# Performance work log

Measured on AMD Instinct MI355X. Metric: run time of the kernel, lower is better.

The kernel has to match this reference:

```python
import jax, jax.numpy as jnp
import numpy as np

D_MODEL = 1024
NUM_HEADS = 16
D_K = D_MODEL // NUM_HEADS


def setup_inputs() -> dict:
    key = jax.random.key(0)
    ks = jax.random.split(key, 9)
    s = 1.0 / np.sqrt(D_MODEL)
    inp = {"x": jax.random.normal(ks[0], (4, 2048, D_MODEL), dtype=jnp.float32)}
    for i, name in enumerate(["q", "k", "v", "o"]):
        inp[f"W_{name}"] = jax.random.uniform(ks[1 + 2 * i], (D_MODEL, D_MODEL), minval=-s, maxval=s, dtype=jnp.float32)
        inp[f"b_{name}"] = jax.random.uniform(ks[2 + 2 * i], (D_MODEL,), minval=-s, maxval=s, dtype=jnp.float32)
    return inp


def reference(x, W_q, b_q, W_k, b_k, W_v, b_v, W_o, b_o):
    B, S, _ = x.shape
    # torch Linear: y = x @ W.T + b ; reshape to [B, H, S, d_k]
    def proj(W, b):
        return (x @ W.T + b).reshape(B, S, NUM_HEADS, D_K).transpose(0, 2, 1, 3)

    Q, K, V = proj(W_q, b_q), proj(W_k, b_k), proj(W_v, b_v)
    scores = jnp.einsum("bhqd,bhkd->bhqk", Q, K) / np.sqrt(D_K).astype(np.float32)
    # additive causal mask: -inf above diagonal
    causal = jnp.triu(jnp.full((S, S), -jnp.inf, dtype=scores.dtype), k=1)
    scores = scores + causal
    attn = jax.nn.softmax(scores, axis=-1)
    attn = jnp.nan_to_num(attn, nan=0.0)
    # dropout is identity in eval mode
    out = jnp.einsum("bhqk,bhkd->bhqd", attn, V)
    out = out.transpose(0, 2, 1, 3).reshape(B, S, D_MODEL)
    return out @ W_o.T + b_o
```

## Files before the change

### kernel.cpp

```cpp
#include <hip/hip_runtime.h>
#include <hip/hip_bf16.h>
#include <stdint.h>

#define D_MODEL 1024
#define SEQ     2048
#define NH      16
#define DK      64
#define PSTR    72

typedef __bf16 bf16x8 __attribute__((ext_vector_type(8)));
typedef float  f32x4  __attribute__((ext_vector_type(4)));
typedef unsigned short u16;

#define CFENCE() asm volatile("" ::: "memory")

__device__ __forceinline__ u16 f2bf(float f) {
    uint32_t u = __float_as_uint(f);
    u += 0x7FFFu + ((u >> 16) & 1u);
    return (u16)(u >> 16);
}

__device__ __forceinline__ void gl2lds16(const u16* g, u16* l) {
    __builtin_amdgcn_global_load_lds(
        (const __attribute__((address_space(1))) uint32_t*)g,
        (__attribute__((address_space(3))) uint32_t*)l, 16, 0, 0);
}

__global__ __launch_bounds__(256) void cvt_kernel(const float* __restrict__ src,
                                                  u16* __restrict__ dst, int n4) {
    int i = blockIdx.x * blockDim.x + threadIdx.x;
    if (i >= n4) return;
    float4 v = reinterpret_cast<const float4*>(src)[i];
    ushort4 o;
    o.x = f2bf(v.x); o.y = f2bf(v.y); o.z = f2bf(v.z); o.w = f2bf(v.w);
    reinterpret_cast<ushort4*>(dst)[i] = o;
}

__global__ __launch_bounds__(256) void cvt4_kernel(
    const float* __restrict__ s0, const float* __restrict__ s1,
    const float* __restrict__ s2, const float* __restrict__ s3,
    u16* __restrict__ d0, u16* __restrict__ d1,
    u16* __restrict__ d2, u16* __restrict__ d3, int n4) {
    int z = blockIdx.y;
    const float* s = (z == 0) ? s0 : (z == 1) ? s1 : (z == 2) ? s2 : s3;
    u16* d = (z == 0) ? d0 : (z == 1) ? d1 : (z == 2) ? d2 : d3;
    int i = blockIdx.x * blockDim.x + threadIdx.x;
    if (i >= n4) return;
    float4 v = reinterpret_cast<const float4*>(s)[i];
    ushort4 o;
    o.x = f2bf(v.x); o.y = f2bf(v.y); o.z = f2bf(v.z); o.w = f2bf(v.w);
    reinterpret_cast<ushort4*>(d)[i] = o;
}

__device__ __forceinline__ void gemm128_body(const u16* __restrict__ Ag,
                                             const u16* __restrict__ Bg,
                                             u16* As, u16* Bs, f32x4 acc[4][4]) {
    const int K = D_MODEL;
    int tid = threadIdx.x, wave = tid >> 6, lane = tid & 63;
    int l15 = lane & 15, quad = lane >> 4;
    int srow = lane >> 2;
    int scol = (lane & 3) * 8;
    int arg4 = (wave >> 1) * 4;
    int brg4 = (wave & 1) * 4;
#pragma unroll 1
    for (int kc = 0; kc < K; kc += 64) {
        __syncthreads();
#pragma unroll
        for (int j = 0; j < 4; ++j) {
            int p = wave * 4 + j;
            int rg = p >> 1, h = p & 1;
            int row = rg * 16 + srow;
            int col = kc + h * 32 + scol;
            gl2lds16(Ag + row * K + col, As + p * 512);
            gl2lds16(Bg + row * K + col, Bs + p * 512);
        }
        __syncthreads();
#pragma unroll
        for (int h = 0; h < 2; ++h) {
            bf16x8 af[4], bfr[4];
#pragma unroll
            for (int s = 0; s < 4; ++s) {
                af[s]  = *reinterpret_cast<const bf16x8*>(
                    As + ((arg4 + s) * 2 + h) * 512 + l15 * 32 + quad * 8);
                bfr[s] = *reinterpret_cast<const bf16x8*>(
                    Bs + ((brg4 + s) * 2 + h) * 512 + l15 * 32 + quad * 8);
            }
#pragma unroll
            for (int ms = 0; ms < 4; ++ms)
#pragma unroll
                for (int ns = 0; ns < 4; ++ns)
                    acc[ms][ns] = __builtin_amdgcn_mfma_f32_16x16x32_bf16(
                        af[ms], bfr[ns], acc[ms][ns], 0, 0, 0);
        }
    }
}

__device__ __forceinline__ void stage_half(const u16* __restrict__ gb, u16* ls,
                                           int w2, int srow, int scol) {
#pragma unroll
    for (int i = 0; i < 2; ++i)
        gl2lds16(gb + ((w2 + i) * 8 + srow) * D_MODEL + scol,
                 ls + (w2 + i) * 512);
}

__global__ __launch_bounds__(512, 2) void qkv_gemm256(
    const u16* __restrict__ xb,
    const u16* __restrict__ Wq, const u16* __restrict__ Wk, const u16* __restrict__ Wv,
    const float* __restrict__ bq, const float* __restrict__ bk, const float* __restrict__ bv,
    u16* __restrict__ qo, u16* __restrict__ ko, u16* __restrict__ vto) {
    __shared__ __align__(16) u16 smA[2][2][8192];
    __shared__ __align__(16) u16 smB[2][2][8192];
    int z = blockIdx.z;
    const u16* W = (z == 0) ? Wq : (z == 1) ? Wk : Wv;
    const float* bias = (z == 0) ? bq : (z == 1) ? bk : bv;
    int tid = threadIdx.x;
    int lane = tid & 63, wave = tid >> 6;
    int l15 = lane & 15, quad = lane >> 4;
    int wr = wave >> 2, wc = wave & 3;
    int w2 = wave * 2;
    const u16* Abase = xb + (size_t)blockIdx.x * 256 * D_MODEL;
    const u16* Bbase = W + (size_t)blockIdx.y * 256 * D_MODEL;

    int srow = lane >> 3;
    int scol = ((lane & 7) ^ (lane >> 3)) * 8;
    int xb_ = (l15 & 7) << 4;
    int c0 = ((quad * 16) ^ xb_) >> 1;
    int c1 = ((64 + quad * 16) ^ xb_) >> 1;
    int rb0 = (wc & 1) * 64;

    f32x4 acc[8][4];
#pragma unroll
    for (int m = 0; m < 8; ++m)
#pragma unroll
        for (int n = 0; n < 4; ++n) acc[m][n] = (f32x4){0.f, 0.f, 0.f, 0.f};

    stage_half(Abase, &smA[0][0][0], w2, srow, scol);
    stage_half(Abase + 128 * D_MODEL, &smA[0][1][0], w2, srow, scol);
    stage_half(Bbase, &smB[0][0][0], w2, srow, scol);
    stage_half(Bbase + 128 * D_MODEL, &smB[0][1][0], w2, srow, scol);
    stage_half(Abase + 64, &smA[1][0][0], w2, srow, scol);
    asm volatile("s_waitcnt vmcnt(2)" ::: "memory");
    __builtin_amdgcn_s_barrier();
    CFENCE();

#pragma unroll 1
    for (int t = 0; t < 16; ++t) {
        const int p = t & 1;
        const u16* As = &smA[p][wr][0];
        const u16* Bs = &smB[p][wc >> 1][0];
        bf16x8 af[4][2], bfr[4][2];

#pragma unroll
        for (int m = 0; m < 4; ++m) {
            af[m][0] = *reinterpret_cast<const bf16x8*>(As + (m * 16 + l15) * 64 + c0);
            af[m][1] = *reinterpret_cast<const bf16x8*>(As + (m * 16 + l15) * 64 + c1);
        }
#pragma unroll
        for (int nn = 0; nn < 2; ++nn) {
            bfr[nn][0] = *reinterpret_cast<const bf16x8*>(Bs + (rb0 + nn * 16 + l15) * 64 + c0);
            bfr[nn][1] = *reinterpret_cast<const bf16x8*>(Bs + (rb0 + nn * 16 + l15) * 64 + c1);
        }
        if (t < 15) stage_half(Abase + 128 * D_MODEL + (t + 1) * 64,
                               &smA[(t + 1) & 1][1][0], w2, srow, scol);
        CFENCE(); __builtin_amdgcn_s_barrier(); CFENCE();
        __builtin_amdgcn_s_setprio(1);
#pragma unroll
        for (int m = 0; m < 4; ++m)
#pragma unroll
            for (int nn = 0; nn < 2; ++nn) {
                acc[m][nn] = __builtin_amdgcn_mfma_f32_16x16x32_bf16(af[m][0], bfr[nn][0], acc[m][nn], 0, 0, 0);
                acc[m][nn] = __builtin_amdgcn_mfma_f32_16x16x32_bf16(af[m][1], bfr[nn][1], acc[m][nn], 0, 0, 0);
            }
        __builtin_amdgcn_s_setprio(0);
        CFENCE(); __builtin_amdgcn_s_barrier(); CFENCE();

#pragma unroll
        for (int nn = 0; nn < 2; ++nn) {
            bfr[2 + nn][0] = *reinterpret_cast<const bf16x8*>(Bs + (rb0 + (2 + nn) * 16 + l15) * 64 + c0);
            bfr[2 + nn][1] = *reinterpret_cast<const bf16x8*>(Bs + (rb0 + (2 + nn) * 16 + l15) * 64 + c1);
        }
        if (t < 15) stage_half(Bbase + (t + 1) * 64,
                               &smB[(t + 1) & 1][0][0], w2, srow, scol);
        CFENCE(); __builtin_amdgcn_s_barrier(); CFENCE();
        __builtin_amdgcn_s_setprio(1);
#pragma unroll
        for (int m = 0; m < 4; ++m)
#pragma unroll
            for (int nn = 0; nn < 2; ++nn) {
                acc[m][2 + nn] = __builtin_amdgcn_mfma_f32_16x16x32_bf16(af[m][0], bfr[2 + nn][0], acc[m][2 + nn], 0, 0, 0);
                acc[m][2 + nn] = __builtin_amdgcn_mfma_f32_16x16x32_bf16(af[m][1], bfr[2 + nn][1], acc[m][2 + nn], 0, 0, 0);
            }
        __builtin_amdgcn_s_setprio(0);
        CFENCE(); __builtin_amdgcn_s_barrier(); CFENCE();

#pragma unroll
        for (int m = 0; m < 4; ++m) {
            af[m][0] = *reinterpret_cast<const bf16x8*>(As + ((m + 4) * 16 + l15) * 64 + c0);
            af[m][1] = *reinterpret_cast<const bf16x8*>(As + ((m + 4) * 16 + l15) * 64 + c1);
        }
        if (t < 15) stage_half(Bbase + 128 * D_MODEL + (t + 1) * 64,
                               &smB[(t + 1) & 1][1][0], w2, srow, scol);
        CFENCE(); __builtin_amdgcn_s_barrier(); CFENCE();
        __builtin_amdgcn_s_setprio(1);
#pragma unroll
        for (int m = 0; m < 4; ++m)
#pragma unroll
            for (int nn = 0; nn < 2; ++nn) {
                acc[4 + m][nn] = __builtin_amdgcn_mfma_f32_16x16x32_bf16(af[m][0], bfr[nn][0], acc[4 + m][nn], 0, 0, 0);
                acc[4 + m][nn] = __builtin_amdgcn_mfma_f32_16x16x32_bf16(af[m][1], bfr[nn][1], acc[4 + m][nn], 0, 0, 0);
            }
        __builtin_amdgcn_s_setprio(0);
        CFENCE(); __builtin_amdgcn_s_barrier(); CFENCE();

        if (t < 14) stage_half(Abase + (t + 2) * 64,
                               &smA[p][0][0], w2, srow, scol);
        CFENCE(); __builtin_amdgcn_s_barrier(); CFENCE();
        __builtin_amdgcn_s_setprio(1);
#pragma unroll
        for (int m = 0; m < 4; ++m)
#pragma unroll
            for (int nn = 0; nn < 2; ++nn) {
                acc[4 + m][2 + nn] = __builtin_amdgcn_mfma_f32_16x16x32_bf16(af[m][0], bfr[2 + nn][0], acc[4 + m][2 + nn], 0, 0, 0);
                acc[4 + m][2 + nn] = __builtin_amdgcn_mfma_f32_16x16x32_bf16(af[m][1], bfr[2 + nn][1], acc[4 + m][2 + nn], 0, 0, 0);
            }
        __builtin_amdgcn_s_setprio(0);
        if (t < 14) {
            asm volatile("s_waitcnt vmcnt(2)" ::: "memory");
            __builtin_amdgcn_s_barrier(); CFENCE();
        } else if (t == 14) {
            asm volatile("s_waitcnt vmcnt(0)" ::: "memory");
            __builtin_amdgcn_s_barrier(); CFENCE();
        }
    }

    int mw = blockIdx.x * 256 + wr * 128;
    int nwb = blockIdx.y * 256 + wc * 64;
    int hq = (nwb >> 6) & (NH - 1);
    const float qscale = 0.125f * 1.4426950408889634f;

    if (z != 2) {
        u16* dst = (z == 0) ? qo : ko;
        float sc = (z == 0) ? qscale : 1.0f;
        u16* tw = &smA[0][0][0] + wave * 1152;
        float bv0 = bias[nwb + 0 * 16 + l15];
        float bv1 = bias[nwb + 1 * 16 + l15];
        float bv2 = bias[nwb + 2 * 16 + l15];
        float bv3 = bias[nwb + 3 * 16 + l15];
#pragma unroll
        for (int mf = 0; mf < 8; ++mf) {
#pragma unroll
            for (int nf = 0; nf < 4; ++nf) {
                int c = nf * 16 + l15;
                float bv_ = (nf == 0) ? bv0 : (nf == 1) ? bv1 : (nf == 2) ? bv2 : bv3;
#pragma unroll
                for (int r = 0; r < 4; ++r) {
                    int w = quad * 4 + r;
                    tw[w * 72 + (((c >> 3) ^ (w & 7)) << 3) + (c & 7)] =
                        f2bf((acc[mf][nf][r] + bv_) * sc);
                }
            }
            asm volatile("s_waitcnt lgkmcnt(0)" ::: "memory");
#pragma unroll
            for (int i = 0; i < 2; ++i) {
                int w = i * 8 + (lane >> 3);
                bf16x8 vv = *reinterpret_cast<const bf16x8*>(
                    tw + w * 72 + (((lane & 7) ^ (w & 7)) << 3));
                int sg = mw + mf * 16 + w;
                int b = sg >> 11, ss = sg & (SEQ - 1);
                *reinterpret_cast<bf16x8*>(
                    &dst[((b * NH + hq) * SEQ + ss) * DK + (lane & 7) * 8]) = vv;
            }
            asm volatile("s_waitcnt lgkmcnt(0)" ::: "memory");
        }
    } else {
        u16* tw = &smA[0][0][0] + wave * 4608;
        float bv0 = bias[nwb + 0 * 16 + l15];
        float bv1 = bias[nwb + 1 * 16 + l15];
        float bv2 = bias[nwb + 2 * 16 + l15];
        float bv3 = bias[nwb + 3 * 16 + l15];
#pragma unroll
        for (int half = 0; half < 2; ++half) {
#pragma unroll
            for (int mfi = 0; mfi < 4; ++mfi) {
                int mf = half * 4 + mfi;
#pragma unroll
                for (int nf = 0; nf < 4; ++nf) {
                    int w = nf * 16 + l15;
                    float bv_ = (nf == 0) ? bv0 : (nf == 1) ? bv1 : (nf == 2) ? bv2 : bv3;
                    int sl = mfi * 16 + quad * 4;
                    ushort4 pk;
                    pk.x = f2bf(acc[mf][nf][0] + bv_);
                    pk.y = f2bf(acc[mf][nf][1] + bv_);
                    pk.z = f2bf(acc[mf][nf][2] + bv_);
                    pk.w = f2bf(acc[mf][nf][3] + bv_);
                    *reinterpret_cast<ushort4*>(
                        tw + w * 72 + (((sl >> 3) ^ (w & 7)) << 3) + (sl & 7)) = pk;
                }
            }
            asm volatile("s_waitcnt lgkmcnt(0)" ::: "memory");
#pragma unroll
            for (int i = 0; i < 8; ++i) {
                int w = i * 8 + (lane >> 3);
                bf16x8 vv = *reinterpret_cast<const bf16x8*>(
                    tw + w * 72 + (((lane & 7) ^ (w & 7)) << 3));
                int sg = mw + half * 64 + (lane & 7) * 8;
                int b = sg >> 11, ss = sg & (SEQ - 1);
                *reinterpret_cast<bf16x8*>(
                    &vto[((b * NH + hq) * DK + w) * SEQ + ss]) = vv;
            }
            asm volatile("s_waitcnt lgkmcnt(0)" ::: "memory");
        }
    }
}

__global__ __launch_bounds__(256) void out_gemm(
    const u16* __restrict__ ab, const u16* __restrict__ Wo,
    const float* __restrict__ bo, float* __restrict__ out) {
    __shared__ __align__(16) u16 As[16 * 512], Bs[16 * 512];
    int lane = threadIdx.x & 63, wave = threadIdx.x >> 6;
    int l15 = lane & 15, quad = lane >> 4;
    int mw = blockIdx.x * 128 + (wave >> 1) * 64;
    int nw = blockIdx.y * 128 + (wave & 1) * 64;

    f32x4 acc[4][4];
#pragma unroll
    for (int ms = 0; ms < 4; ++ms)
#pragma unroll
        for (int ns = 0; ns < 4; ++ns)
            acc[ms][ns] = (f32x4){0.f, 0.f, 0.f, 0.f};

    gemm128_body(ab + blockIdx.x * 128 * D_MODEL, Wo + blockIdx.y * 128 * D_MODEL,
                 As, Bs, acc);

#pragma unroll
    for (int ns = 0; ns < 4; ++ns) {
        int n = nw + ns * 16 + l15;
        float bv_ = bo[n];
#pragma unroll
        for (int ms = 0; ms < 4; ++ms) {
            int mbase = mw + ms * 16 + quad * 4;
#pragma unroll
            for (int r = 0; r < 4; ++r)
                out[(mbase + r) * D_MODEL + n] = acc[ms][ns][r] + bv_;
        }
    }
}

__global__ __launch_bounds__(256, 3) void attn_kernel(
    const u16* __restrict__ Q, const u16* __restrict__ Kc,
    const u16* __restrict__ Vt, u16* __restrict__ ao) {
    __shared__ __align__(16) u16 Ks[2][8 * 512], Vs[2][8 * 512], Plds[4][32 * PSTR];
    int t = 15 - blockIdx.x, bh = blockIdx.y;
    int lane = threadIdx.x & 63, wave = threadIdx.x >> 6;
    int l15 = lane & 15, quad = lane >> 4;
    const u16* Qb = Q + bh * (SEQ * DK);
    const u16* Kb = Kc + bh * (SEQ * DK);
    const u16* Vb = Vt + bh * (DK * SEQ);
    int b = bh >> 4, hh = bh & 15;
    u16* Pw = &Plds[wave][0];

    int q0w = t * 128 + wave * 32;
    int qmax = q0w + 31;

    bf16x8 qf[2][2];
#pragma unroll
    for (int nf = 0; nf < 2; ++nf)
#pragma unroll
        for (int h = 0; h < 2; ++h)
            qf[nf][h] = *reinterpret_cast<const bf16x8*>(
                Qb + (q0w + nf * 16 + l15) * DK + h * 32 + quad * 8);

    f32x4 o[2][4];
#pragma unroll
    for (int ma = 0; ma < 2; ++ma)
#pragma unroll
        for (int nf = 0; nf < 4; ++nf)
            o[ma][nf] = (f32x4){0.f, 0.f, 0.f, 0.f};
    float lsum[2] = {0.f, 0.f};

    int nch = 2 * t + 2;

#pragma unroll
    for (int h = 0; h < 2; ++h) {
        gl2lds16(Kb + (wave * 16 + l15) * DK + h * 32 + quad * 8,
                 &Ks[0][(wave * 2 + h) * 512]);
        gl2lds16(Vb + (wave * 16 + l15) * SEQ + h * 32 + quad * 8,
                 &Vs[0][(wave * 2 + h) * 512]);
    }

#pragma unroll 1
    for (int c = 0; c < nch; ++c) {
        int k0 = c * 64;
        int cur = c & 1;
        CFENCE(); __builtin_amdgcn_s_barrier(); CFENCE();
        if (c + 1 < nch) {
            int k1 = k0 + 64;
#pragma unroll
            for (int h = 0; h < 2; ++h) {
                gl2lds16(Kb + (k1 + wave * 16 + l15) * DK + h * 32 + quad * 8,
                         &Ks[cur ^ 1][(wave * 2 + h) * 512]);
                gl2lds16(Vb + (wave * 16 + l15) * SEQ + k1 + h * 32 + quad * 8,
                         &Vs[cur ^ 1][(wave * 2 + h) * 512]);
            }
            asm volatile("s_waitcnt vmcnt(4)" ::: "memory");
        } else {
            asm volatile("s_waitcnt vmcnt(0)" ::: "memory");
        }
        CFENCE(); __builtin_amdgcn_s_barrier(); CFENCE();
        if (k0 > qmax) continue;

        const u16* Kcur = &Ks[cur][0];
        const u16* Vcur = &Vs[cur][0];

        f32x4 s[4][2];
#pragma unroll
        for (int mf = 0; mf < 4; ++mf) {
            bf16x8 kf0 = *reinterpret_cast<const bf16x8*>(Kcur + (mf * 2 + 0) * 512 + lane * 8);
            bf16x8 kf1 = *reinterpret_cast<const bf16x8*>(Kcur + (mf * 2 + 1) * 512 + lane * 8);
#pragma unroll
            for (int nf = 0; nf < 2; ++nf) {
                f32x4 z = (f32x4){0.f, 0.f, 0.f, 0.f};
                z = __builtin_amdgcn_mfma_f32_16x16x32_bf16(kf0, qf[nf][0], z, 0, 0, 0);
                z = __builtin_amdgcn_mfma_f32_16x16x32_bf16(kf1, qf[nf][1], z, 0, 0, 0);
                s[mf][nf] = z;
            }
        }
        if (k0 + 63 > q0w) {
#pragma unroll
            for (int mf = 0; mf < 4; ++mf) {
                int key = k0 + mf * 16 + quad * 4;
#pragma unroll
                for (int nf = 0; nf < 2; ++nf) {
                    int q = q0w + nf * 16 + l15;
#pragma unroll
                    for (int r = 0; r < 4; ++r)
                        if (key + r > q) s[mf][nf][r] = -__builtin_inff();
                }
            }
        }
#pragma unroll
        for (int mf = 0; mf < 4; ++mf)
#pragma unroll
            for (int nf = 0; nf < 2; ++nf) {
                float p0 = __builtin_amdgcn_exp2f(s[mf][nf][0]);
                float p1 = __builtin_amdgcn_exp2f(s[mf][nf][1]);
                float p2 = __builtin_amdgcn_exp2f(s[mf][nf][2]);
                float p3 = __builtin_amdgcn_exp2f(s[mf][nf][3]);
                lsum[nf] += (p0 + p1) + (p2 + p3);
                ushort4 pk;
                pk.x = f2bf(p0); pk.y = f2bf(p1); pk.z = f2bf(p2); pk.w = f2bf(p3);
                *reinterpret_cast<ushort4*>(
                    Pw + (nf * 16 + l15) * PSTR + mf * 16 + quad * 4) = pk;
            }
        __asm__ volatile("s_waitcnt lgkmcnt(0)" ::: "memory");
        bf16x8 pa[2][2];
#pragma unroll
        for (int ma = 0; ma < 2; ++ma)
#pragma unroll
            for (int h = 0; h < 2; ++h)
                pa[ma][h] = *reinterpret_cast<const bf16x8*>(
                    Pw + (ma * 16 + l15) * PSTR + h * 32 + quad * 8);
#pragma unroll
        for (int nf = 0; nf < 4; ++nf) {
            bf16x8 vf0 = *reinterpret_cast<const bf16x8*>(Vcur + (nf * 2 + 0) * 512 + lane * 8);
            bf16x8 vf1 = *reinterpret_cast<const bf16x8*>(Vcur + (nf * 2 + 1) * 512 + lane * 8);
#pragma unroll
            for (int ma = 0; ma < 2; ++ma) {
                o[ma][nf] = __builtin_amdgcn_mfma_f32_16x16x32_bf16(pa[ma][0], vf0, o[ma][nf], 0, 0, 0);
                o[ma][nf] = __builtin_amdgcn_mfma_f32_16x16x32_bf16(pa[ma][1], vf1, o[ma][nf], 0, 0, 0);
            }
        }
    }
    lsum[0] += __shfl_xor(lsum[0], 16);
    lsum[0] += __shfl_xor(lsum[0], 32);
    lsum[1] += __shfl_xor(lsum[1], 16);
    lsum[1] += __shfl_xor(lsum[1], 32);
#pragma unroll
    for (int ma = 0; ma < 2; ++ma) {
#pragma unroll
        for (int r = 0; r < 4; ++r) {
            float inv = __builtin_amdgcn_rcpf(__shfl(lsum[ma], quad * 4 + r));
            int q = q0w + ma * 16 + quad * 4 + r;
#pragma unroll
            for (int nf = 0; nf < 4; ++nf) {
                int d = nf * 16 + l15;
                ao[(b * SEQ + q) * D_MODEL + hh * DK + d] = f2bf(o[ma][nf][r] * inv);
            }
        }
    }
}

extern "C" void kernel_launch(void* const* d_in, const int* in_sizes, int n_in,
                              void* d_out, int out_size, void* d_ws, size_t ws_size,
                              hipStream_t stream) {
    const float* x  = (const float*)d_in[0];
    const float* Wq = (const float*)d_in[1];
    const float* bq = (const float*)d_in[2];
    const float* Wk = (const float*)d_in[3];
    const float* bk = (const float*)d_in[4];
    const float* Wv = (const float*)d_in[5];
    const float* bv = (const float*)d_in[6];
    const float* Wo = (const float*)d_in[7];
    const float* bo = (const float*)d_in[8];
    float* out = (float*)d_out;
    char* ws = (char*)d_ws;

    const size_t XB = 16777216;
    const size_t WB = 2097152;
    u16* xb  = (u16*)(ws);
    u16* wqb = (u16*)(ws + XB);
    u16* wkb = (u16*)(ws + XB + WB);
    u16* wvb = (u16*)(ws + XB + 2 * WB);
    u16* wob = (u16*)(ws + XB + 3 * WB);
    u16* qb  = (u16*)(ws + XB + 4 * WB);
    u16* kb  = (u16*)(ws + 2 * XB + 4 * WB);
    u16* vtb = (u16*)(ws + 3 * XB + 4 * WB);
    u16* ab  = (u16*)(ws + 4 * XB + 4 * WB);

    cvt_kernel<<<8192, 256, 0, stream>>>(x, xb, 2097152);
    cvt4_kernel<<<dim3(1024, 4), 256, 0, stream>>>(Wq, Wk, Wv, Wo,
                                                   wqb, wkb, wvb, wob, 262144);

    qkv_gemm256<<<dim3(32, 4, 3), 512, 0, stream>>>(xb, wqb, wkb, wvb, bq, bk, bv,
                                                    qb, kb, vtb);
    attn_kernel<<<dim3(16, 64), 256, 0, stream>>>(qb, kb, vtb, ab);
    out_gemm<<<dim3(64, 8), 256, 0, stream>>>(ab, wob, bo, out);
}
```

Baseline: 308.9 us.

## Enlarge attention blocks to 256 queries with XCD-aware head mapping

The attention kernel now uses 512-thread blocks covering 256 query rows, so each K/V chunk staged in LDS is shared by eight waves instead of four, halving K/V reload traffic per query. The grid is flattened to 512 blocks, with a mapping that keeps eight heads on each XCD for L2 locality and interleaves heavy and light causal tiles for load balance. Each wave now issues one K and one V load per chunk, so the wait count changes accordingly. In exchange the blocks are coarser, there are fewer of them, and the causal work per block is less uniform, which may leave CUs idle at the tail.

```diff
diff --git a/kernel.cpp b/kernel.cpp
--- a/kernel.cpp
+++ b/kernel.cpp
@@ -346,11 +346,15 @@
     }
 }
 
-__global__ __launch_bounds__(256, 3) void attn_kernel(
+__global__ __launch_bounds__(512, 4) void attn_kernel(
     const u16* __restrict__ Q, const u16* __restrict__ Kc,
     const u16* __restrict__ Vt, u16* __restrict__ ao) {
-    __shared__ __align__(16) u16 Ks[2][8 * 512], Vs[2][8 * 512], Plds[4][32 * PSTR];
-    int t = 15 - blockIdx.x, bh = blockIdx.y;
+    __shared__ __align__(16) u16 Ks[2][8 * 512], Vs[2][8 * 512], Plds[8][32 * PSTR];
+    int id = blockIdx.x;
+    int xcd = id & 7, j = id >> 3;
+    int bh = xcd * 8 + (j & 7);
+    int g = j >> 3;
+    int T = (g & 1) ? (g >> 1) : (7 - (g >> 1));
     int lane = threadIdx.x & 63, wave = threadIdx.x >> 6;
     int l15 = lane & 15, quad = lane >> 4;
     const u16* Qb = Q + bh * (SEQ * DK);
@@ -358,8 +362,9 @@
     const u16* Vb = Vt + bh * (DK * SEQ);
     int b = bh >> 4, hh = bh & 15;
     u16* Pw = &Plds[wave][0];
-
-    int q0w = t * 128 + wave * 32;
+    int wg = wave >> 1, wh = wave & 1;
+
+    int q0w = T * 256 + wave * 32;
     int qmax = q0w + 31;
 
     bf16x8 qf[2][2];
@@ -378,15 +383,10 @@
             o[ma][nf] = (f32x4){0.f, 0.f, 0.f, 0.f};
     float lsum[2] = {0.f, 0.f};
 
-    int nch = 2 * t + 2;
-
-#pragma unroll
-    for (int h = 0; h < 2; ++h) {
-        gl2lds16(Kb + (wave * 16 + l15) * DK + h * 32 + quad * 8,
-                 &Ks[0][(wave * 2 + h) * 512]);
-        gl2lds16(Vb + (wave * 16 + l15) * SEQ + h * 32 + quad * 8,
-                 &Vs[0][(wave * 2 + h) * 512]);
-    }
+    int nch = 4 * T + 4;
+
+    gl2lds16(Kb + (wg * 16 + l15) * DK + wh * 32 + quad * 8, &Ks[0][wave * 512]);
+    gl2lds16(Vb + (wg * 16 + l15) * SEQ + wh * 32 + quad * 8, &Vs[0][wave * 512]);
 
 #pragma unroll 1
     for (int c = 0; c < nch; ++c) {
@@ -395,14 +395,11 @@
         CFENCE(); __builtin_amdgcn_s_barrier(); CFENCE();
         if (c + 1 < nch) {
             int k1 = k0 + 64;
-#pragma unroll
-            for (int h = 0; h < 2; ++h) {
-                gl2lds16(Kb + (k1 + wave * 16 + l15) * DK + h * 32 + quad * 8,
-                         &Ks[cur ^ 1][(wave * 2 + h) * 512]);
-                gl2lds16(Vb + (wave * 16 + l15) * SEQ + k1 + h * 32 + quad * 8,
-                         &Vs[cur ^ 1][(wave * 2 + h) * 512]);
-            }
-            asm volatile("s_waitcnt vmcnt(4)" ::: "memory");
+            gl2lds16(Kb + (k1 + wg * 16 + l15) * DK + wh * 32 + quad * 8,
+                     &Ks[cur ^ 1][wave * 512]);
+            gl2lds16(Vb + (wg * 16 + l15) * SEQ + k1 + wh * 32 + quad * 8,
+                     &Vs[cur ^ 1][wave * 512]);
+            asm volatile("s_waitcnt vmcnt(2)" ::: "memory");
         } else {
             asm volatile("s_waitcnt vmcnt(0)" ::: "memory");
         }
@@ -523,6 +520,6 @@
 
     qkv_gemm256<<<dim3(32, 4, 3), 512, 0, stream>>>(xb, wqb, wkb, wvb, bq, bk, bv,
                                                     qb, kb, vtb);
-    attn_kernel<<<dim3(16, 64), 256, 0, stream>>>(qb, kb, vtb, ab);
+    attn_kernel<<<512, 512, 0, stream>>>(qb, kb, vtb, ab);
     out_gemm<<<dim3(64, 8), 256, 0, stream>>>(ab, wob, bo, out);
 }
```

After: 269.2 us. 1.15x faster.
